# Kernel tuning notes

Hardware: AMD Instinct MI355X
Metric: run time of the kernel (lower is better)

The kernel has to match this reference:

```python
import jax, jax.numpy as jnp
import numpy as np

B, L, E, H = 512, 32, 2048, 32
D = E // H  # 64


def setup_inputs() -> dict:
    key = jax.random.key(0)
    ks = jax.random.split(key, 10)
    s = 0.02
    return {
        "x": jax.random.normal(ks[0], (B, L, E), dtype=jnp.float32),
        "wq": jax.random.normal(ks[1], (E, E), dtype=jnp.float32) * s,
        "bq": jnp.zeros((E,), dtype=jnp.float32),
        "wk": jax.random.normal(ks[2], (E, E), dtype=jnp.float32) * s,
        "bk": jnp.zeros((E,), dtype=jnp.float32),
        "wv": jax.random.normal(ks[3], (E, E), dtype=jnp.float32) * s,
        "bv": jnp.zeros((E,), dtype=jnp.float32),
        "wo": jax.random.normal(ks[4], (E, E), dtype=jnp.float32) * s,
        "bo": jnp.zeros((E,), dtype=jnp.float32),
        "rel_pos_enc": jax.random.normal(ks[5], (2 * 32 - 1, D), dtype=jnp.float32),
    }


def reference(x, wq, bq, wk, bk, wv, bv, wo, bo, rel_pos_enc):
    b, l, e = x.shape
    h, d = H, D
    scale = d ** -0.5
    # projections (torch Linear: x @ W.T + b)
    q = (x @ wq.T + bq).reshape(b, l, h, d).transpose(0, 2, 1, 3)  # [B,H,L,D]
    k = (x @ wk.T + bk).reshape(b, l, h, d).transpose(0, 2, 1, 3)
    v = (x @ wv.T + bv).reshape(b, l, h, d).transpose(0, 2, 1, 3)
    scores = jnp.einsum("bhid,bhjd->bhij", q, k) * scale  # [B,H,L,L]
    # relative position gather: idx[i,j] = i - j + (L-1) in [0, 2L-2]
    pos = jnp.arange(l)
    rel_idx = pos[:, None] - pos[None, :] + (l - 1)
    rel_pos = rel_pos_enc[rel_idx]  # [L,L,D]
    # faithful to torch broadcasted matmul (batch dims (B,H) vs (L,), H==L):
    # rel_score[b,h,i,j] = sum_d q[b,h,i,d] * rel_pos[h,j,d]
    scores = scores + jnp.einsum("bhid,hjd->bhij", q, rel_pos)
    attn = jax.nn.softmax(scores, axis=-1)  # dropout p=0 (eval)
    out = jnp.einsum("bhij,bhjd->bhid", attn, v)  # [B,H,L,D]
    out = out.transpose(0, 2, 1, 3).reshape(b, l, e)
    return out @ wo.T + bo
```

## Files before the change

kernel.cpp:

```cpp
#include <hip/hip_runtime.h>
#include <hip/hip_bf16.h>
#include <stdint.h>

typedef __bf16 bf16x8 __attribute__((ext_vector_type(8)));
typedef float f32x4 __attribute__((ext_vector_type(4)));
typedef unsigned short u16x8 __attribute__((ext_vector_type(8)));
typedef unsigned short u16x4 __attribute__((ext_vector_type(4)));

#define G_AS __attribute__((address_space(1)))
#define L_AS __attribute__((address_space(3)))

__device__ __forceinline__ void gload_lds16(const void* g, void* l) {
  __builtin_amdgcn_global_load_lds((G_AS void*)g, (L_AS void*)l, 16, 0, 0);
}

__device__ __forceinline__ float b2f(unsigned short u) {
  union { float f; unsigned int i; } cv;
  cv.i = ((unsigned int)u) << 16;
  return cv.f;
}

__device__ __forceinline__ unsigned short f2b(float f) {
  unsigned int u = __float_as_uint(f);
  unsigned int r = u + 0x7FFFu + ((u >> 16) & 1u);
  return (unsigned short)(r >> 16);
}


__global__ void k_cast_f32_bf16(const float* __restrict__ src,
                                unsigned short* __restrict__ dst, int n4) {
  int i = blockIdx.x * blockDim.x + threadIdx.x;
  if (i >= n4) return;
  float4 v = reinterpret_cast<const float4*>(src)[i];
  u16x4 o;
  o[0] = f2b(v.x); o[1] = f2b(v.y); o[2] = f2b(v.z); o[3] = f2b(v.w);
  reinterpret_cast<u16x4*>(dst)[i] = o;
}

__global__ void k_build_wqkv(const float* __restrict__ wq, const float* __restrict__ wk,
                             const float* __restrict__ wv, unsigned short* __restrict__ dst) {
  int i = blockIdx.x * blockDim.x + threadIdx.x;
  if (i >= 3145728) return;
  int e = i << 2;
  int row = e >> 11;
  int col = e & 2047;
  const float* src; float sc = 1.0f;
  if (row < 2048) { src = wq + ((size_t)row << 11); }
  else if (row < 4096) { src = wk + ((size_t)(row - 2048) << 11); sc = 0.125f; }
  else { src = wv + ((size_t)(row - 4096) << 11); }
  float4 v = *reinterpret_cast<const float4*>(src + col);
  u16x4 o;
  o[0] = f2b(v.x * sc); o[1] = f2b(v.y * sc); o[2] = f2b(v.z * sc); o[3] = f2b(v.w * sc);
  *reinterpret_cast<u16x4*>(dst + e) = o;
}

__global__ void k_build_bqkv(const float* __restrict__ bq, const float* __restrict__ bk,
                             const float* __restrict__ bv, float* __restrict__ dst) {
  int i = blockIdx.x * blockDim.x + threadIdx.x;
  if (i >= 6144) return;
  float v;
  if (i < 2048) v = bq[i];
  else if (i < 4096) v = bk[i - 2048] * 0.125f;
  else v = bv[i - 4096];
  dst[i] = v;
}

__global__ void k_build_rel(const float* __restrict__ rpe, unsigned short* __restrict__ dst) {
  int i = blockIdx.x * blockDim.x + threadIdx.x;
  if (i >= 16384) return;
  int h = i >> 9;
  int j = (i >> 4) & 31;
  int d = (i & 15) << 2;
  const float* s = rpe + (size_t)(h - j + 31) * 64 + d;
  float4 v = *reinterpret_cast<const float4*>(s);
  u16x4 o;
  o[0] = f2b(v.x); o[1] = f2b(v.y); o[2] = f2b(v.z); o[3] = f2b(v.w);
  *reinterpret_cast<u16x4*>(dst + ((size_t)i << 2)) = o;
}


template <int OUT_F32>
__global__ __launch_bounds__(512, 1)
void k_gemm256(const unsigned short* __restrict__ A,
               const unsigned short* __restrict__ B,
               const float* __restrict__ bias,
               void* __restrict__ Cptr,
               int M, int N, int K)
{
  __shared__ __align__(16) unsigned short As[3][8192];
  __shared__ __align__(16) unsigned short Bs[3][8192];

  const int nbn = N >> 8;
  const int cpx = gridDim.x >> 3;
  const int orig = blockIdx.x;
  const int wg = (orig & 7) * cpx + (orig >> 3);
  const int bm = wg / nbn;
  const int bn = wg % nbn;

  const int tid = threadIdx.x;
  const int lane = tid & 63;
  const int wid = tid >> 6;
  const int wr = wid >> 2;
  const int wc = wid & 3;

  const int rs = tid >> 2;
  const int cs = ((tid & 3) ^ ((tid >> 3) & 3)) << 3;
  const unsigned short* agA0 = A + (size_t)(bm * 256 + rs) * K + cs;
  const unsigned short* agA1 = agA0 + (size_t)128 * K;
  const unsigned short* agB0 = B + (size_t)(bn * 256 + rs) * K + cs;
  const unsigned short* agB1 = agB0 + (size_t)128 * K;
  const int ldst = tid * 8;

  const int fr = lane & 15;
  const int q  = lane >> 4;
  const int sx = q ^ ((fr >> 1) & 3);
  const int rbase = fr * 32 + sx * 8;
  const int aOff = wr * 4096 + rbase;
  const int bOff = wc * 2048 + rbase;

  f32x4 acc[8][4] = {};
  const int NT = K >> 5;

#pragma unroll
  for (int pf = 0; pf < 2; ++pf) {
    const int kof = pf << 5;
    gload_lds16(agA0 + kof, &As[pf][ldst]);
    gload_lds16(agA1 + kof, &As[pf][ldst + 4096]);
    gload_lds16(agB0 + kof, &Bs[pf][ldst]);
    gload_lds16(agB1 + kof, &Bs[pf][ldst + 4096]);
  }
  asm volatile("s_waitcnt vmcnt(4)" ::: "memory");
  asm volatile("s_barrier" ::: "memory");

  int rb = 0;
  int sb = 2;
  for (int t = 0; t < NT; ++t) {
    const unsigned short* ab = &As[rb][0];
    const unsigned short* bb = &Bs[rb][0];
    const bool st = (t + 2) < NT;
    const int kof = (t + 2) << 5;

    bf16x8 afL[4], bf[4];
#pragma unroll
    for (int n = 0; n < 4; ++n)
      bf[n] = *reinterpret_cast<const bf16x8*>(bb + bOff + n * 512);
#pragma unroll
    for (int m = 0; m < 4; ++m)
      afL[m] = *reinterpret_cast<const bf16x8*>(ab + aOff + m * 512);
    if (st) {
      gload_lds16(agA0 + kof, &As[sb][ldst]);
      gload_lds16(agA1 + kof, &As[sb][ldst + 4096]);
    }
    __builtin_amdgcn_s_setprio(1);
#pragma unroll
    for (int m = 0; m < 4; ++m)
#pragma unroll
      for (int n = 0; n < 4; ++n)
        acc[m][n] = __builtin_amdgcn_mfma_f32_16x16x32_bf16(afL[m], bf[n], acc[m][n], 0, 0, 0);
    __builtin_amdgcn_s_setprio(0);

    bf16x8 afH[4];
#pragma unroll
    for (int m = 0; m < 4; ++m)
      afH[m] = *reinterpret_cast<const bf16x8*>(ab + aOff + (4 + m) * 512);
    if (st) {
      gload_lds16(agB0 + kof, &Bs[sb][ldst]);
      gload_lds16(agB1 + kof, &Bs[sb][ldst + 4096]);
    }
    __builtin_amdgcn_s_setprio(1);
#pragma unroll
    for (int m = 0; m < 4; ++m)
#pragma unroll
      for (int n = 0; n < 4; ++n)
        acc[4 + m][n] = __builtin_amdgcn_mfma_f32_16x16x32_bf16(afH[m], bf[n], acc[4 + m][n], 0, 0, 0);
    __builtin_amdgcn_s_setprio(0);

    if (t < NT - 2)       asm volatile("s_waitcnt vmcnt(4)" ::: "memory");
    else if (t == NT - 2) asm volatile("s_waitcnt vmcnt(0)" ::: "memory");
    __builtin_amdgcn_sched_barrier(0);
    asm volatile("s_barrier" ::: "memory");
    __builtin_amdgcn_sched_barrier(0);

    rb = (rb == 2) ? 0 : rb + 1;
    sb = (sb == 2) ? 0 : sb + 1;
  }

  const int rBase = bm * 256 + wr * 128 + (q << 2);
  const int cBase = bn * 256 + wc * 64 + fr;
#pragma unroll
  for (int n = 0; n < 4; ++n) {
    const int col = cBase + n * 16;
    const float bv = bias[col];
#pragma unroll
    for (int m = 0; m < 8; ++m) {
      const int row = rBase + m * 16;
#pragma unroll
      for (int r = 0; r < 4; ++r) {
        float v = acc[m][n][r] + bv;
        if (OUT_F32) {
          reinterpret_cast<float*>(Cptr)[(size_t)(row + r) * N + col] = v;
        } else {
          reinterpret_cast<unsigned short*>(Cptr)[(size_t)(row + r) * N + col] = f2b(v);
        }
      }
    }
  }
}


__global__ __launch_bounds__(256)
void k_attn(const unsigned short* __restrict__ qkv,
            const unsigned short* __restrict__ relb,
            unsigned short* __restrict__ ctx)
{
  __shared__ __align__(16) unsigned short qS[4][32 * 72];
  __shared__ __align__(16) unsigned short krS[4][32 * 72];
  __shared__ __align__(16) unsigned short vTS[4][64 * 40];
  __shared__ __align__(16) unsigned short pS[4][32 * 40];

  const int w = threadIdx.x >> 6;
  const int lane = threadIdx.x & 63;
  const int b = blockIdx.x >> 3;
  const int h = ((blockIdx.x & 7) << 2) + w;

  const int r = lane >> 1;
  const int d0 = (lane & 1) << 5;
  const unsigned short* base = qkv + (size_t)(b * 32 + r) * 6144 + h * 64 + d0;
  const unsigned short* relp = relb + (((size_t)(h * 32 + r)) << 6) + d0;

  u16x8 uq[4], uk[4], uv[4], ur[4];
#pragma unroll
  for (int c = 0; c < 4; ++c) {
    uq[c] = *reinterpret_cast<const u16x8*>(base + 8 * c);
    uk[c] = *reinterpret_cast<const u16x8*>(base + 2048 + 8 * c);
    uv[c] = *reinterpret_cast<const u16x8*>(base + 4096 + 8 * c);
    ur[c] = *reinterpret_cast<const u16x8*>(relp + 8 * c);
  }
#pragma unroll
  for (int c = 0; c < 4; ++c) {
    *reinterpret_cast<u16x8*>(&qS[w][r * 72 + d0 + 8 * c]) = uq[c];
    u16x8 kr;
#pragma unroll
    for (int e = 0; e < 8; ++e) kr[e] = f2b(b2f(uk[c][e]) + b2f(ur[c][e]));
    *reinterpret_cast<u16x8*>(&krS[w][r * 72 + d0 + 8 * c]) = kr;
#pragma unroll
    for (int e = 0; e < 8; ++e) vTS[w][(d0 + 8 * c + e) * 40 + r] = uv[c][e];
  }
  asm volatile("s_waitcnt lgkmcnt(0)" ::: "memory");
  __builtin_amdgcn_sched_barrier(0);

  const int fr16 = lane & 15;
  const int qq = lane >> 4;
  f32x4 accs[2][2] = {};
#pragma unroll
  for (int ks = 0; ks < 2; ++ks) {
    bf16x8 aq[2], bk[2];
#pragma unroll
    for (int m = 0; m < 2; ++m)
      aq[m] = *reinterpret_cast<const bf16x8*>(&qS[w][(16 * m + fr16) * 72 + 32 * ks + qq * 8]);
#pragma unroll
    for (int n = 0; n < 2; ++n)
      bk[n] = *reinterpret_cast<const bf16x8*>(&krS[w][(16 * n + fr16) * 72 + 32 * ks + qq * 8]);
#pragma unroll
    for (int m = 0; m < 2; ++m)
#pragma unroll
      for (int n = 0; n < 2; ++n)
        accs[m][n] = __builtin_amdgcn_mfma_f32_16x16x32_bf16(aq[m], bk[n], accs[m][n], 0, 0, 0);
  }

#pragma unroll
  for (int m = 0; m < 2; ++m) {
#pragma unroll
    for (int rr = 0; rr < 4; ++rr) {
      float a0 = accs[m][0][rr], a1 = accs[m][1][rr];
      float mx = fmaxf(a0, a1);
      mx = fmaxf(mx, __shfl_xor(mx, 1));
      mx = fmaxf(mx, __shfl_xor(mx, 2));
      mx = fmaxf(mx, __shfl_xor(mx, 4));
      mx = fmaxf(mx, __shfl_xor(mx, 8));
      float p0 = __expf(a0 - mx), p1 = __expf(a1 - mx);
      float sm = p0 + p1;
      sm += __shfl_xor(sm, 1);
      sm += __shfl_xor(sm, 2);
      sm += __shfl_xor(sm, 4);
      sm += __shfl_xor(sm, 8);
      const float inv = 1.0f / sm;
      const int i = 16 * m + qq * 4 + rr;
      pS[w][i * 40 + fr16]      = f2b(p0 * inv);
      pS[w][i * 40 + 16 + fr16] = f2b(p1 * inv);
    }
  }
  asm volatile("s_waitcnt lgkmcnt(0)" ::: "memory");
  __builtin_amdgcn_sched_barrier(0);

  bf16x8 ap[2], bv[4];
#pragma unroll
  for (int m = 0; m < 2; ++m)
    ap[m] = *reinterpret_cast<const bf16x8*>(&pS[w][(16 * m + fr16) * 40 + qq * 8]);
#pragma unroll
  for (int n = 0; n < 4; ++n)
    bv[n] = *reinterpret_cast<const bf16x8*>(&vTS[w][(16 * n + fr16) * 40 + qq * 8]);
  f32x4 acco[2][4] = {};
#pragma unroll
  for (int m = 0; m < 2; ++m)
#pragma unroll
    for (int n = 0; n < 4; ++n)
      acco[m][n] = __builtin_amdgcn_mfma_f32_16x16x32_bf16(ap[m], bv[n], acco[m][n], 0, 0, 0);

#pragma unroll
  for (int m = 0; m < 2; ++m) {
#pragma unroll
    for (int rr = 0; rr < 4; ++rr) {
      const int i = 16 * m + qq * 4 + rr;
      unsigned short* orow = ctx + (size_t)(b * 32 + i) * 2048 + h * 64;
#pragma unroll
      for (int n = 0; n < 4; ++n)
        orow[16 * n + fr16] = f2b(acco[m][n][rr]);
    }
  }
}


extern "C" void kernel_launch(void* const* d_in, const int* in_sizes, int n_in,
                              void* d_out, int out_size, void* d_ws, size_t ws_size,
                              hipStream_t stream) {
  const float* x   = (const float*)d_in[0];
  const float* wq  = (const float*)d_in[1];
  const float* bq  = (const float*)d_in[2];
  const float* wk  = (const float*)d_in[3];
  const float* bk  = (const float*)d_in[4];
  const float* wv  = (const float*)d_in[5];
  const float* bv  = (const float*)d_in[6];
  const float* wo  = (const float*)d_in[7];
  const float* bo  = (const float*)d_in[8];
  const float* rpe = (const float*)d_in[9];

  char* ws = (char*)d_ws;
  unsigned short* xb    = (unsigned short*)(ws);
  unsigned short* wqkvb = (unsigned short*)(ws + 67108864);
  unsigned short* wob   = (unsigned short*)(ws + 67108864 + 25165824);
  unsigned short* qkvb  = (unsigned short*)(ws + 67108864 + 25165824 + 8388608);
  float*          bqkv  = (float*)(ws + 67108864 + 25165824 + 8388608 + 201326592);
  unsigned short* relb  = (unsigned short*)(ws + 67108864 + 25165824 + 8388608 + 201326592 + 24576);

  k_cast_f32_bf16<<<32768, 256, 0, stream>>>(x, xb, 8388608);
  k_build_wqkv<<<12288, 256, 0, stream>>>(wq, wk, wv, wqkvb);
  k_cast_f32_bf16<<<4096, 256, 0, stream>>>(wo, wob, 1048576);
  k_build_bqkv<<<24, 256, 0, stream>>>(bq, bk, bv, bqkv);
  k_build_rel<<<64, 256, 0, stream>>>(rpe, relb);

  k_gemm256<0><<<(16384 / 256) * (6144 / 256), 512, 0, stream>>>(
      xb, wqkvb, bqkv, qkvb, 16384, 6144, 2048);

  k_attn<<<4096, 256, 0, stream>>>(qkvb, relb, xb);

  k_gemm256<1><<<(16384 / 256) * (2048 / 256), 512, 0, stream>>>(
      xb, wob, bo, (float*)d_out, 16384, 2048, 2048);
}
```

Measured before the change: 704.6 us.

## Switch GEMM to BK=64 double-buffered LDS pipeline with 8-way XOR swizzle

Changes the GEMM main loop from three LDS buffers with a K-tile of 32 to two buffers with a K-tile of 64. Each tile is loaded as four 64-row chunks with an 8-way XOR column swizzle, and fragments are read at offset and offset^32 to cover both K halves. This halves the number of barrier and waitcnt round-trips per K and doubles the MFMA work per iteration. The trade-off is shallower prefetch (one tile ahead, waiting with vmcnt(0)), so global load latency may be less hidden.

```diff
diff --git a/kernel.cpp b/kernel.cpp
--- a/kernel.cpp
+++ b/kernel.cpp
@@ -87,8 +87,8 @@
                void* __restrict__ Cptr,
                int M, int N, int K)
 {
-  __shared__ __align__(16) unsigned short As[3][8192];
-  __shared__ __align__(16) unsigned short Bs[3][8192];
+  __shared__ __align__(16) unsigned short As[2][16384];
+  __shared__ __align__(16) unsigned short Bs[2][16384];
 
   const int nbn = N >> 8;
   const int cpx = gridDim.x >> 3;
@@ -103,86 +103,92 @@
   const int wr = wid >> 2;
   const int wc = wid & 3;
 
-  const int rs = tid >> 2;
-  const int cs = ((tid & 3) ^ ((tid >> 3) & 3)) << 3;
-  const unsigned short* agA0 = A + (size_t)(bm * 256 + rs) * K + cs;
-  const unsigned short* agA1 = agA0 + (size_t)128 * K;
-  const unsigned short* agB0 = B + (size_t)(bn * 256 + rs) * K + cs;
-  const unsigned short* agB1 = agB0 + (size_t)128 * K;
+  const int r0 = tid >> 3;
+  const int cs = ((tid & 7) ^ ((tid >> 3) & 7)) << 3;
+  const unsigned short* agA = A + (size_t)(bm * 256 + r0) * K + cs;
+  const unsigned short* agB = B + (size_t)(bn * 256 + r0) * K + cs;
   const int ldst = tid * 8;
 
   const int fr = lane & 15;
   const int q  = lane >> 4;
-  const int sx = q ^ ((fr >> 1) & 3);
-  const int rbase = fr * 32 + sx * 8;
-  const int aOff = wr * 4096 + rbase;
-  const int bOff = wc * 2048 + rbase;
+  const int sx0 = q ^ (fr & 7);
+  const int aBase = (wr * 128 + fr) * 64 + sx0 * 8;
+  const int bBase = (wc * 64 + fr) * 64 + sx0 * 8;
 
   f32x4 acc[8][4] = {};
-  const int NT = K >> 5;
-
-#pragma unroll
-  for (int pf = 0; pf < 2; ++pf) {
-    const int kof = pf << 5;
-    gload_lds16(agA0 + kof, &As[pf][ldst]);
-    gload_lds16(agA1 + kof, &As[pf][ldst + 4096]);
-    gload_lds16(agB0 + kof, &Bs[pf][ldst]);
-    gload_lds16(agB1 + kof, &Bs[pf][ldst + 4096]);
-  }
-  asm volatile("s_waitcnt vmcnt(4)" ::: "memory");
+  const int NT = K >> 6;
+
+#pragma unroll
+  for (int j = 0; j < 4; ++j)
+    gload_lds16(agA + (size_t)(64 * j) * K, &As[0][ldst + 4096 * j]);
+#pragma unroll
+  for (int j = 0; j < 4; ++j)
+    gload_lds16(agB + (size_t)(64 * j) * K, &Bs[0][ldst + 4096 * j]);
+  asm volatile("s_waitcnt vmcnt(0)" ::: "memory");
   asm volatile("s_barrier" ::: "memory");
 
-  int rb = 0;
-  int sb = 2;
   for (int t = 0; t < NT; ++t) {
+    const int rb = t & 1;
+    const int sb = rb ^ 1;
     const unsigned short* ab = &As[rb][0];
     const unsigned short* bb = &Bs[rb][0];
-    const bool st = (t + 2) < NT;
-    const int kof = (t + 2) << 5;
-
-    bf16x8 afL[4], bf[4];
-#pragma unroll
-    for (int n = 0; n < 4; ++n)
-      bf[n] = *reinterpret_cast<const bf16x8*>(bb + bOff + n * 512);
-#pragma unroll
-    for (int m = 0; m < 4; ++m)
-      afL[m] = *reinterpret_cast<const bf16x8*>(ab + aOff + m * 512);
+    const bool st = (t + 1) < NT;
+    const int kof = (t + 1) << 6;
+
     if (st) {
-      gload_lds16(agA0 + kof, &As[sb][ldst]);
-      gload_lds16(agA1 + kof, &As[sb][ldst + 4096]);
+#pragma unroll
+      for (int j = 0; j < 4; ++j)
+        gload_lds16(agA + (size_t)(64 * j) * K + kof, &As[sb][ldst + 4096 * j]);
+    }
+
+    bf16x8 bf[4][2], af[4][2];
+#pragma unroll
+    for (int n = 0; n < 4; ++n) {
+      bf[n][0] = *reinterpret_cast<const bf16x8*>(bb + (bBase + n * 1024));
+      bf[n][1] = *reinterpret_cast<const bf16x8*>(bb + ((bBase + n * 1024) ^ 32));
+    }
+#pragma unroll
+    for (int m = 0; m < 4; ++m) {
+      af[m][0] = *reinterpret_cast<const bf16x8*>(ab + (aBase + m * 1024));
+      af[m][1] = *reinterpret_cast<const bf16x8*>(ab + ((aBase + m * 1024) ^ 32));
     }
     __builtin_amdgcn_s_setprio(1);
 #pragma unroll
-    for (int m = 0; m < 4; ++m)
-#pragma unroll
-      for (int n = 0; n < 4; ++n)
-        acc[m][n] = __builtin_amdgcn_mfma_f32_16x16x32_bf16(afL[m], bf[n], acc[m][n], 0, 0, 0);
+    for (int ks = 0; ks < 2; ++ks)
+#pragma unroll
+      for (int m = 0; m < 4; ++m)
+#pragma unroll
+        for (int n = 0; n < 4; ++n)
+          acc[m][n] = __builtin_amdgcn_mfma_f32_16x16x32_bf16(af[m][ks], bf[n][ks], acc[m][n], 0, 0, 0);
     __builtin_amdgcn_s_setprio(0);
 
-    bf16x8 afH[4];
-#pragma unroll
-    for (int m = 0; m < 4; ++m)
-      afH[m] = *reinterpret_cast<const bf16x8*>(ab + aOff + (4 + m) * 512);
+    bf16x8 afH[4][2];
+#pragma unroll
+    for (int m = 0; m < 4; ++m) {
+      afH[m][0] = *reinterpret_cast<const bf16x8*>(ab + (aBase + (4 + m) * 1024));
+      afH[m][1] = *reinterpret_cast<const bf16x8*>(ab + ((aBase + (4 + m) * 1024) ^ 32));
+    }
     if (st) {
-      gload_lds16(agB0 + kof, &Bs[sb][ldst]);
-      gload_lds16(agB1 + kof, &Bs[sb][ldst + 4096]);
+#pragma unroll
+      for (int j = 0; j < 4; ++j)
+        gload_lds16(agB + (size_t)(64 * j) * K + kof, &Bs[sb][ldst + 4096 * j]);
     }
     __builtin_amdgcn_s_setprio(1);
 #pragma unroll
-    for (int m = 0; m < 4; ++m)
-#pragma unroll
-      for (int n = 0; n < 4; ++n)
-        acc[4 + m][n] = __builtin_amdgcn_mfma_f32_16x16x32_bf16(afH[m], bf[n], acc[4 + m][n], 0, 0, 0);
+    for (int ks = 0; ks < 2; ++ks)
+#pragma unroll
+      for (int m = 0; m < 4; ++m)
+#pragma unroll
+        for (int n = 0; n < 4; ++n)
+          acc[4 + m][n] = __builtin_amdgcn_mfma_f32_16x16x32_bf16(afH[m][ks], bf[n][ks], acc[4 + m][n], 0, 0, 0);
     __builtin_amdgcn_s_setprio(0);
 
-    if (t < NT - 2)       asm volatile("s_waitcnt vmcnt(4)" ::: "memory");
-    else if (t == NT - 2) asm volatile("s_waitcnt vmcnt(0)" ::: "memory");
-    __builtin_amdgcn_sched_barrier(0);
-    asm volatile("s_barrier" ::: "memory");
-    __builtin_amdgcn_sched_barrier(0);
-
-    rb = (rb == 2) ? 0 : rb + 1;
-    sb = (sb == 2) ? 0 : sb + 1;
+    if (st) {
+      asm volatile("s_waitcnt vmcnt(0)" ::: "memory");
+      __builtin_amdgcn_sched_barrier(0);
+      asm volatile("s_barrier" ::: "memory");
+      __builtin_amdgcn_sched_barrier(0);
+    }
   }
 
   const int rBase = bm * 256 + wr * 128 + (q << 2);
```

New measurement: 703.6 us. Within noise of the previous version (-0.1%).
